# Performance work log

Measured on AMD Instinct MI355X. Metric: run time of the kernel, lower is better.

Reference implementation:

```python
import jax, jax.numpy as jnp
import numpy as np

EPS = 1e-8


def setup_inputs() -> dict:
    key = jax.random.key(0)
    k1, k2 = jax.random.split(key)
    N, F, K, C = 16384, 64, 32, 100
    membership = jax.random.uniform(k1, (N, F, K), dtype=jnp.float32)
    teacher_probs = jax.random.uniform(k2, (N, C), dtype=jnp.float32)
    return {"membership": membership, "teacher_probs": teacher_probs}


def reference(membership, teacher_probs):
    # membership: [N, F, K]  soft bin assignments per feature
    # teacher_probs: [N, C]  teacher class distribution per sample
    N, F, K = membership.shape
    bin_mass = membership.sum(axis=0) + EPS  # [F, K]
    # Contraction form of (membership[:, :, :, None] * teacher_probs[:, None, None, :]).sum(0)
    # avoids the N*F*K*C intermediate.
    centroids = jnp.einsum('nfk,nc->fkc', membership, teacher_probs) / bin_mass[:, :, None]  # [F, K, C]
    # Intra-bin: minimize entropy of each bin's class distribution, mass-weighted.
    intra_entropy = -jnp.sum(centroids * jnp.log(centroids + EPS), axis=2)  # [F, K]
    loss_intra = jnp.sum(intra_entropy * bin_mass) / N
    # Inter-bin: maximize entropy of the mixture of adjacent bins
    # (loss_inter is negative entropy summed, added with +0.5 weight).
    mixture = 0.5 * (centroids[:, :-1, :] + centroids[:, 1:, :])  # [F, K-1, C]
    loss_inter = jnp.sum(mixture * jnp.log(mixture + EPS))
    return loss_intra + 0.5 * loss_inter
```

## Files before the change

### kernel.cpp

```cpp
#include <hip/hip_runtime.h>
#include <hip/hip_bf16.h>

#define NS   16384
#define FKD  2048
#define CD   100
#define CP   112
#define NKC  32
#define PHASES 16
#define EPSF 1e-8f
#define SFK  (FKD * CP)
#define NGRP (NS / 8)

typedef float f32x4 __attribute__((ext_vector_type(4)));
typedef short bf16x8 __attribute__((ext_vector_type(8)));

__device__ inline unsigned short f2bf(float f) {
    unsigned int u = __float_as_uint(f);
    u += 0x7FFFu + ((u >> 16) & 1u);
    return (unsigned short)(u >> 16);
}

__device__ __forceinline__ void gload16(const float* g, const float* l) {
    __builtin_amdgcn_global_load_lds(
        (const __attribute__((address_space(1))) void*)g,
        (__attribute__((address_space(3))) void*)l, 16, 0, 0);
}

__global__ __launch_bounds__(256) void ebl_prep(
    const float* __restrict__ tp, unsigned short* __restrict__ Bp,
    unsigned* __restrict__ cnt)
{
    const int idx = blockIdx.x * 256 + threadIdx.x;
    if (idx == 0) *cnt = 0;
    if (idx >= NGRP * CP) return;
    const int g = idx / CP, c = idx - g * CP;
    unsigned short v[8];
    if (c < CD) {
        const float* p = tp + (size_t)g * 8 * CD + c;
        #pragma unroll
        for (int j = 0; j < 8; ++j) v[j] = f2bf(p[(size_t)j * CD]);
    } else {
        const unsigned short fill = (c == CD) ? 0x3F80 : 0;
        #pragma unroll
        for (int j = 0; j < 8; ++j) v[j] = fill;
    }
    *reinterpret_cast<uint4*>(Bp + (size_t)idx * 8) = *reinterpret_cast<const uint4*>(v);
}

__global__ __launch_bounds__(128) void ebl_gemm(
    const float* __restrict__ mem, const unsigned short* __restrict__ Bp,
    unsigned short* __restrict__ spart)
{
    __shared__ float At[3 * 2 * 2048];

    const int t  = threadIdx.x;
    const int w  = t >> 6;
    const int l  = t & 63;
    const int lg = l >> 4, lr = l & 15;
    const int m0 = blockIdx.x * 128;
    const int kc = blockIdx.y;
    const int n0 = kc * (PHASES * 32);
    const int gb = n0 >> 3;

    const float* gbase = mem + (size_t)(n0 + lg) * FKD + (m0 + w * 64 + lr * 4);

    f32x4 acc[4][7];
    #pragma unroll
    for (int i = 0; i < 4; ++i)
        #pragma unroll
        for (int nt = 0; nt < 7; ++nt) acc[i][nt] = (f32x4){0.f, 0.f, 0.f, 0.f};

    bf16x8 b0[7], b1[7];
    int o0 = (0 * 2 + w) * 2048, o1 = (1 * 2 + w) * 2048, o2 = (2 * 2 + w) * 2048;

#define SB() __builtin_amdgcn_sched_barrier(0)
#define STAGE(bo, p) { \
    const float* gs = gbase + (size_t)(p) * 32 * FKD; \
    _Pragma("unroll") \
    for (int q = 0; q < 8; ++q) \
        gload16(gs + (size_t)q * 4 * FKD, At + (bo) + q * 256); \
    SB(); }
#define LOADB(dst, p) { \
    const unsigned short* bq = Bp + ((size_t)(gb + (p) * 4 + lg) * CP + lr) * 8; \
    _Pragma("unroll") \
    for (int nt = 0; nt < 7; ++nt) dst[nt] = *reinterpret_cast<const bf16x8*>(bq + nt * 128); \
    SB(); }
#define WAITV(n) { asm volatile("s_waitcnt vmcnt(" #n ")" ::: "memory"); SB(); }
#define COMPUTE(bo, bB) { \
    bf16x8 af[4]; \
    _Pragma("unroll") \
    for (int i = 0; i < 4; ++i) \
        _Pragma("unroll") \
        for (int j = 0; j < 8; ++j) { \
            float v = At[(bo) + (2 * lg + (j >> 2)) * 256 + (j & 3) * 64 + i * 16 + lr]; \
            af[i][j] = (short)f2bf(v); } \
    _Pragma("unroll") \
    for (int i = 0; i < 4; ++i) \
        _Pragma("unroll") \
        for (int nt = 0; nt < 7; ++nt) \
            acc[i][nt] = __builtin_amdgcn_mfma_f32_16x16x32_bf16(af[i], bB[nt], acc[i][nt], 0, 0, 0); }

    STAGE(o0, 0)
    LOADB(b0, 0)
    STAGE(o1, 1)

    for (int ph = 0; ph < PHASES - 2; ph += 2) {
        LOADB(b1, ph + 1)
        STAGE(o2, ph + 2)
        WAITV(23)
        COMPUTE(o0, b0)
        LOADB(b0, ph + 2)
        STAGE(o0, ph + 3)
        WAITV(23)
        COMPUTE(o1, b1)
        const int tmp = o2; o2 = o1; o1 = o0; o0 = tmp;
    }
    LOADB(b1, PHASES - 1)
    WAITV(15)
    COMPUTE(o0, b0)
    WAITV(0)
    COMPUTE(o1, b1)

#undef SB
#undef STAGE
#undef LOADB
#undef WAITV
#undef COMPUTE

    unsigned short* sp = spart + (size_t)kc * SFK;
    #pragma unroll
    for (int i = 0; i < 4; ++i) {
        #pragma unroll
        for (int nt = 0; nt < 7; ++nt) {
            const int c = nt * 16 + lr;
            #pragma unroll
            for (int r = 0; r < 4; ++r) {
                const int mm = m0 + w * 64 + i * 16 + lg * 4 + r;
                sp[(size_t)mm * CP + c] = f2bf(acc[i][nt][r]);
            }
        }
    }
}

__global__ __launch_bounds__(256) void ebl_tail(
    const unsigned short* __restrict__ spart, float* __restrict__ fpart,
    unsigned* __restrict__ cnt, float* __restrict__ out)
{
    __shared__ float Ss[32 * CP];
    __shared__ float massL[32];
    __shared__ float red[4];
    __shared__ int lastFlag;
    const int t = threadIdx.x;
    const int f = blockIdx.x;
    const size_t base = (size_t)f * 32 * CP;

    for (int v = t; v < 32 * CP / 8; v += 256) {
        float s[8];
        #pragma unroll
        for (int j = 0; j < 8; ++j) s[j] = 0.f;
        for (int p = 0; p < NKC; ++p) {
            uint4 raw = *reinterpret_cast<const uint4*>(spart + (size_t)p * SFK + base + (size_t)v * 8);
            const unsigned short* u = reinterpret_cast<const unsigned short*>(&raw);
            #pragma unroll
            for (int j = 0; j < 8; ++j) s[j] += __uint_as_float((unsigned)u[j] << 16);
        }
        #pragma unroll
        for (int j = 0; j < 8; ++j) Ss[v * 8 + j] = s[j];
    }
    __syncthreads();
    if (t < 32) massL[t] = Ss[t * CP + CD] + EPSF;
    __syncthreads();

    float a_int = 0.f, a_mix = 0.f;
    for (int idx = t; idx < 32 * CD; idx += 256) {
        const int k = idx / CD, c = idx - k * CD;
        const float cent = Ss[k * CP + c] / massL[k];
        a_int -= cent * logf(cent + EPSF) * massL[k];
    }
    for (int idx = t; idx < 31 * CD; idx += 256) {
        const int k = idx / CD, c = idx - k * CD;
        const float mix = 0.5f * (Ss[k * CP + c] / massL[k] + Ss[(k + 1) * CP + c] / massL[k + 1]);
        a_mix += mix * logf(mix + EPSF);
    }

    float part = a_int * (1.0f / (float)NS) + 0.5f * a_mix;
    #pragma unroll
    for (int off = 32; off > 0; off >>= 1) part += __shfl_down(part, off);
    if ((t & 63) == 0) red[t >> 6] = part;
    __syncthreads();

    if (t == 0) {
        fpart[f] = (red[0] + red[1]) + (red[2] + red[3]);
        __threadfence();
        const unsigned ticket =
            __hip_atomic_fetch_add(cnt, 1u, __ATOMIC_ACQ_REL, __HIP_MEMORY_SCOPE_AGENT);
        lastFlag = (ticket == 63);
    }
    __syncthreads();

    if (lastFlag && t < 64) {
        float v = __hip_atomic_load(&fpart[t], __ATOMIC_ACQUIRE, __HIP_MEMORY_SCOPE_AGENT);
        #pragma unroll
        for (int off = 32; off > 0; off >>= 1) v += __shfl_down(v, off);
        if (t == 0) out[0] = v;
    }
}

extern "C" void kernel_launch(void* const* d_in, const int* in_sizes, int n_in,
                              void* d_out, int out_size, void* d_ws, size_t ws_size,
                              hipStream_t stream)
{
    const float* mem = (const float*)d_in[0];
    const float* tp  = (const float*)d_in[1];
    float* out = (float*)d_out;

    const size_t bpBytes = (size_t)NGRP * CP * 8 * 2;

    unsigned short* Bp    = (unsigned short*)d_ws;
    unsigned short* spart = (unsigned short*)((char*)d_ws + bpBytes);
    float*          fpart = (float*)((char*)spart + (size_t)NKC * SFK * 2);
    unsigned*       cnt   = (unsigned*)(fpart + 64);

    ebl_prep<<<(NGRP * CP + 255) / 256, 256, 0, stream>>>(tp, Bp, cnt);
    dim3 grid(FKD / 128, NKC);
    ebl_gemm<<<grid, 128, 0, stream>>>(mem, Bp, spart);
    ebl_tail<<<64, 256, 0, stream>>>(spart, fpart, cnt, out);
}
```

Measured before the change: 51.92 us.

## Halve GEMM M-tile, deepen LDS pipeline to four stages, use packed bf16 convert

The GEMM block now covers 64 feature-bin rows instead of 128, so the grid has twice as many blocks, and each wave holds half the accumulators. The A-staging ring grows from three to four buffers, with buffer indices computed from the phase and a single-phase loop that prefetches three stages ahead. The fp32-to-bf16 conversion now uses the hardware v_cvt_pk_bf16_f32 instruction in place of the manual rounding. The aim is more parallelism, deeper latency hiding and cheaper conversion, at the cost of less B-operand reuse per block and extra register copies of B between phases.

Result: no change. 52.61 us (+1.3%).

```diff
diff --git a/kernel.cpp b/kernel.cpp
--- a/kernel.cpp
+++ b/kernel.cpp
@@ -10,9 +10,11 @@
 #define EPSF 1e-8f
 #define SFK  (FKD * CP)
 #define NGRP (NS / 8)
+#define WBUF 1024
 
 typedef float f32x4 __attribute__((ext_vector_type(4)));
 typedef short bf16x8 __attribute__((ext_vector_type(8)));
+typedef unsigned uint4v __attribute__((ext_vector_type(4)));
 
 __device__ inline unsigned short f2bf(float f) {
     unsigned int u = __float_as_uint(f);
@@ -51,34 +53,35 @@
     const float* __restrict__ mem, const unsigned short* __restrict__ Bp,
     unsigned short* __restrict__ spart)
 {
-    __shared__ float At[3 * 2 * 2048];
+    __shared__ float At[4 * 2 * WBUF];
 
     const int t  = threadIdx.x;
     const int w  = t >> 6;
     const int l  = t & 63;
     const int lg = l >> 4, lr = l & 15;
-    const int m0 = blockIdx.x * 128;
+    const int m0 = blockIdx.x * 64;
     const int kc = blockIdx.y;
     const int n0 = kc * (PHASES * 32);
     const int gb = n0 >> 3;
 
-    const float* gbase = mem + (size_t)(n0 + lg) * FKD + (m0 + w * 64 + lr * 4);
-
-    f32x4 acc[4][7];
-    #pragma unroll
-    for (int i = 0; i < 4; ++i)
+    const float* gbase = mem + (size_t)(n0 + (l >> 3)) * FKD + (m0 + w * 32 + (l & 7) * 4);
+
+    f32x4 acc[2][7];
+    #pragma unroll
+    for (int i = 0; i < 2; ++i)
         #pragma unroll
         for (int nt = 0; nt < 7; ++nt) acc[i][nt] = (f32x4){0.f, 0.f, 0.f, 0.f};
 
     bf16x8 b0[7], b1[7];
-    int o0 = (0 * 2 + w) * 2048, o1 = (1 * 2 + w) * 2048, o2 = (2 * 2 + w) * 2048;
 
 #define SB() __builtin_amdgcn_sched_barrier(0)
-#define STAGE(bo, p) { \
+#define BUFO(p) ((((p) & 3) * 2 + w) * WBUF)
+#define STAGE(p) { \
     const float* gs = gbase + (size_t)(p) * 32 * FKD; \
-    _Pragma("unroll") \
-    for (int q = 0; q < 8; ++q) \
-        gload16(gs + (size_t)q * 4 * FKD, At + (bo) + q * 256); \
+    const int bo_ = BUFO(p); \
+    _Pragma("unroll") \
+    for (int q = 0; q < 4; ++q) \
+        gload16(gs + (size_t)q * 8 * FKD, At + bo_ + q * 256); \
     SB(); }
 #define LOADB(dst, p) { \
     const unsigned short* bq = Bp + ((size_t)(gb + (p) * 4 + lg) * CP + lr) * 8; \
@@ -86,42 +89,55 @@
     for (int nt = 0; nt < 7; ++nt) dst[nt] = *reinterpret_cast<const bf16x8*>(bq + nt * 128); \
     SB(); }
 #define WAITV(n) { asm volatile("s_waitcnt vmcnt(" #n ")" ::: "memory"); SB(); }
-#define COMPUTE(bo, bB) { \
-    bf16x8 af[4]; \
-    _Pragma("unroll") \
-    for (int i = 0; i < 4; ++i) \
+#define COMPUTE(p, bB) { \
+    const int bo_ = BUFO(p); \
+    bf16x8 af[2]; \
+    _Pragma("unroll") \
+    for (int i = 0; i < 2; ++i) { \
+        uint4v u; \
         _Pragma("unroll") \
-        for (int j = 0; j < 8; ++j) { \
-            float v = At[(bo) + (2 * lg + (j >> 2)) * 256 + (j & 3) * 64 + i * 16 + lr]; \
-            af[i][j] = (short)f2bf(v); } \
-    _Pragma("unroll") \
-    for (int i = 0; i < 4; ++i) \
+        for (int jj = 0; jj < 4; ++jj) { \
+            float f0 = At[bo_ + ((2 * lg + (jj >> 1)) * 4 + 2 * (jj & 1))     * 32 + i * 16 + lr]; \
+            float f1 = At[bo_ + ((2 * lg + (jj >> 1)) * 4 + 2 * (jj & 1) + 1) * 32 + i * 16 + lr]; \
+            unsigned uu; \
+            asm("v_cvt_pk_bf16_f32 %0, %1, %2" : "=v"(uu) : "v"(f0), "v"(f1)); \
+            u[jj] = uu; \
+        } \
+        af[i] = __builtin_bit_cast(bf16x8, u); \
+    } \
+    SB(); \
+    _Pragma("unroll") \
+    for (int i = 0; i < 2; ++i) \
         _Pragma("unroll") \
         for (int nt = 0; nt < 7; ++nt) \
             acc[i][nt] = __builtin_amdgcn_mfma_f32_16x16x32_bf16(af[i], bB[nt], acc[i][nt], 0, 0, 0); }
 
-    STAGE(o0, 0)
+    STAGE(0)
+    STAGE(1)
     LOADB(b0, 0)
-    STAGE(o1, 1)
-
-    for (int ph = 0; ph < PHASES - 2; ph += 2) {
+    STAGE(2)
+
+    for (int ph = 0; ph < PHASES - 3; ++ph) {
         LOADB(b1, ph + 1)
-        STAGE(o2, ph + 2)
-        WAITV(23)
-        COMPUTE(o0, b0)
-        LOADB(b0, ph + 2)
-        STAGE(o0, ph + 3)
-        WAITV(23)
-        COMPUTE(o1, b1)
-        const int tmp = o2; o2 = o1; o1 = o0; o0 = tmp;
-    }
+        STAGE(ph + 3)
+        WAITV(15)
+        COMPUTE(ph, b0)
+        #pragma unroll
+        for (int nt = 0; nt < 7; ++nt) b0[nt] = b1[nt];
+    }
+    LOADB(b1, PHASES - 2)
+    WAITV(11)
+    COMPUTE(PHASES - 3, b0)
+    #pragma unroll
+    for (int nt = 0; nt < 7; ++nt) b0[nt] = b1[nt];
     LOADB(b1, PHASES - 1)
-    WAITV(15)
-    COMPUTE(o0, b0)
+    WAITV(7)
+    COMPUTE(PHASES - 2, b0)
     WAITV(0)
-    COMPUTE(o1, b1)
+    COMPUTE(PHASES - 1, b1)
 
 #undef SB
+#undef BUFO
 #undef STAGE
 #undef LOADB
 #undef WAITV
@@ -129,13 +145,13 @@
 
     unsigned short* sp = spart + (size_t)kc * SFK;
     #pragma unroll
-    for (int i = 0; i < 4; ++i) {
+    for (int i = 0; i < 2; ++i) {
         #pragma unroll
         for (int nt = 0; nt < 7; ++nt) {
             const int c = nt * 16 + lr;
             #pragma unroll
             for (int r = 0; r < 4; ++r) {
-                const int mm = m0 + w * 64 + i * 16 + lg * 4 + r;
+                const int mm = m0 + w * 32 + i * 16 + lg * 4 + r;
                 sp[(size_t)mm * CP + c] = f2bf(acc[i][nt][r]);
             }
         }
@@ -222,7 +238,7 @@
     unsigned*       cnt   = (unsigned*)(fpart + 64);
 
     ebl_prep<<<(NGRP * CP + 255) / 256, 256, 0, stream>>>(tp, Bp, cnt);
-    dim3 grid(FKD / 128, NKC);
+    dim3 grid(FKD / 64, NKC);
     ebl_gemm<<<grid, 128, 0, stream>>>(mem, Bp, spart);
     ebl_tail<<<64, 256, 0, stream>>>(spart, fpart, cnt, out);
 }
```
